# Kernel tuning notes

Measured on AMD Instinct MI355X. Metric: run time of the kernel, lower is better.

The kernel has to match this reference:

```python
import jax, jax.numpy as jnp
import numpy as np

B, L, DIM = 4, 2048, 256
NSETS, PP, POSP, LTMP = 4, 4, 16, 16
PI = float(np.pi)


def setup_inputs() -> dict:
    key = jax.random.key(0)
    ks = jax.random.split(key, 8)
    d = DIM
    return {
        "x": jax.random.normal(ks[0], (B, L, d), jnp.float32),
        "key_proj": jax.random.normal(ks[1], (d, NSETS * PP), jnp.float32) / np.sqrt(d),
        "query_proj": jax.random.normal(ks[2], (d, NSETS * PP), jnp.float32) / np.sqrt(d),
        "ltm_key_proj": jax.random.normal(ks[3], (3 * d, LTMP), jnp.float32) / np.sqrt(3 * d),
        "pos_freqs": jnp.exp(jnp.arange(POSP, dtype=jnp.float32) * (-np.log(10000.0) / POSP)),
        "w_value": jax.random.normal(ks[4], (d, d), jnp.float32) / np.sqrt(d),
        "b_value": jnp.zeros(d, jnp.float32),
        "w_ltm_val": jax.random.normal(ks[5], (d, d), jnp.float32) / np.sqrt(d),
        "b_ltm_val": jnp.zeros(d, jnp.float32),
        "ln_gamma": jnp.ones(d, jnp.float32),
        "ln_beta": jnp.zeros(d, jnp.float32),
        "w_out": jax.random.normal(ks[6], (d, d), jnp.float32) / np.sqrt(d),
        "b_out": jnp.zeros(d, jnp.float32),
        "set_weights": jnp.ones(NSETS, jnp.float32),
        "pos_weight": jnp.ones(1, jnp.float32),
        "surprise_scale": jnp.array(5.0, jnp.float32),
        "surprise_bias": jnp.array(0.0, jnp.float32),
        "resonance_scale": jnp.array(5.0, jnp.float32),
        "resonance_threshold": jnp.array(0.3, jnp.float32),
        "ltm_weight": jnp.array(0.5, jnp.float32),
        "ltm_binding_memory": jnp.zeros((LTMP, d), jnp.complex64),
        "ltm_count": jnp.array(0.0, jnp.float32),
    }


def reference(x, key_proj, query_proj, ltm_key_proj, pos_freqs, w_value, b_value,
              w_ltm_val, b_ltm_val, ln_gamma, ln_beta, w_out, b_out, set_weights,
              pos_weight, surprise_scale, surprise_bias, resonance_scale,
              resonance_threshold, ltm_weight, ltm_binding_memory, ltm_count):
    Bx, Lx, D = x.shape
    # phasor encodings
    key_ph = jnp.exp(1j * (jnp.tanh(x @ key_proj) * PI)).reshape(Bx, Lx, NSETS, PP)
    qry_ph = jnp.exp(1j * (jnp.tanh(x @ query_proj) * PI)).reshape(Bx, Lx, NSETS, PP)
    V_real = x @ w_value + b_value
    weights = jax.nn.softmax(set_weights)
    # joint (cross-bank) phasors
    jk = jnp.prod(key_ph, axis=2)   # [B,L,PP]
    jq = jnp.prod(qry_ph, axis=2)
    # exclusive cumsum of joint keys -> resonance-based surprise write gate
    km = jnp.concatenate([jnp.zeros_like(jk[:, :1]), jnp.cumsum(jk[:, :-1], axis=1)], axis=1)
    rmag = jnp.abs(km * jnp.conj(jq)).mean(-1, keepdims=True)
    posf = jnp.maximum(jnp.arange(Lx, dtype=jnp.float32), 1.0)
    nres = rmag / jnp.sqrt(posf)[None, :, None]
    sc = jnp.clip(resonance_scale, 1.0, 20.0)
    th = jnp.clip(resonance_threshold, 0.1, 0.9)
    surprise = 0.5 * (1.0 - jnp.tanh(sc * (nres - th)))
    gate = jax.nn.sigmoid(surprise_scale * (surprise - 0.5) + surprise_bias)
    Vg = (V_real * gate).astype(jnp.complex64)
    # cross-bank holographic memory (joint key binding)
    cross = jnp.real((jnp.cumsum(jk[..., None] * Vg[:, :, None, :], axis=1)
                      * jnp.conj(jq)[..., None]).sum(2))
    # per-bank holographic memory over all planes
    bound_all = key_ph[..., None] * Vg[:, :, None, None, :]            # [B,L,S,P,D]
    mem_all = jnp.cumsum(bound_all.reshape(Bx, Lx, NSETS * PP, D), axis=1)
    mem_all = mem_all.reshape(Bx, Lx, NSETS, PP, D)
    per_bank = jnp.real((mem_all * jnp.conj(qry_ph)[..., None]).sum(3))  # [B,L,S,D]
    total = (per_bank * weights[None, None, :, None]).sum(2)
    total = (total + cross) / (NSETS + 1.0)
    # positional phasor memory (ungated V)
    pos_ph = jnp.exp(1j * (jnp.arange(Lx, dtype=jnp.float32)[:, None] * pos_freqs * 2.0 * PI))  # [L,P]
    Vc = V_real.astype(jnp.complex64)
    ret_pos = jnp.real((jnp.cumsum(pos_ph[None, :, :, None] * Vc[:, :, None, :], axis=1)
                        * jnp.conj(pos_ph)[None, :, :, None]).sum(2))
    total = 0.5 * total + 0.5 * (jax.nn.sigmoid(pos_weight) * ret_pos)  # fixed_gate = 0.5
    # LTM retrieval from persistent binding memory (detached buffers)
    p1 = jnp.arange(1, Lx + 1, dtype=jnp.float32)[None, :, None]
    rm = jnp.cumsum(x, axis=1) / p1
    rv = jnp.cumsum(x * x, axis=1) / p1 - rm * rm
    rs = jnp.sqrt(jnp.clip(rv, 1e-8, None))
    ltm_ph = jnp.exp(1j * (jnp.tanh(jnp.concatenate([x, rm, rs], -1) @ ltm_key_proj) * PI))  # [B,L,LTMP]
    pers = jnp.real((ltm_binding_memory[None, None] * jnp.conj(ltm_ph)[..., None]).sum(2))
    pnorm = jnp.sqrt(jnp.maximum(ltm_count, 1.0) * LTMP)
    total = total + jax.nn.sigmoid(ltm_weight) * (pers / pnorm)
    # output: LayerNorm + Linear on normalized retrieval, residual
    nrm = jnp.sqrt(jnp.arange(1, Lx + 1, dtype=jnp.float32) * PP)[None, :, None]
    h = total / nrm
    mu = h.mean(-1, keepdims=True)
    var = ((h - mu) ** 2).mean(-1, keepdims=True)
    hn = (h - mu) / jnp.sqrt(var + 1e-5) * ln_gamma + ln_beta
    return x + hn @ w_out + b_out
```

## Files before the change

kernel.cpp:

```cpp
#include <hip/hip_runtime.h>
#include <math.h>

#define B 4
#define L 2048
#define D 256
#define POSP 16
#define LTMP 16
#define T 64
#define C 32
#define F 72
#define PI_F 3.14159274101257324f
#define TWO_PI_D 6.283185307179586476925286766559

__global__ __launch_bounds__(256) void pos_kernel(const float* __restrict__ pos_freqs,
                                                  float* __restrict__ posc,
                                                  float* __restrict__ poss) {
    int idx = blockIdx.x * 256 + threadIdx.x;
    if (idx >= L * POSP) return;
    int t = idx >> 4, p = idx & 15;
    float a = (float)t * pos_freqs[p];
    float th = (a * 2.0f) * PI_F;
    double r = fmod((double)th, TWO_PI_D);
    posc[idx] = (float)cos(r);
    poss[idx] = (float)sin(r);
}

__global__ __launch_bounds__(256) void featurize_kernel(
    const float* __restrict__ x, const float* __restrict__ key_proj,
    const float* __restrict__ query_proj, const float* __restrict__ w_value,
    const float* __restrict__ b_value, const float* __restrict__ set_weights,
    float* __restrict__ V, float* __restrict__ fk, float* __restrict__ fq,
    float* __restrict__ partial) {
    int cg = blockIdx.x;
    int rc = blockIdx.y;
    int b  = blockIdx.z;
    int row0 = rc * 64;
    int tid = threadIdx.x;
    __shared__ float xs[2][32][74];
    __shared__ float ws[2][32][84];
    __shared__ float zbuf[64][20];
    __shared__ float jkv[64][9];
    const bool has_proj = (cg < 2);
    const float* proj = (cg == 0) ? key_proj : query_proj;
    int rg = tid >> 4, cgi = tid & 15;
    int r0 = rg * 4, c0 = cgi * 4;
    int prow = tid >> 2, pc4 = tid & 3;
    float acc[4][4], accp[4];
#pragma unroll
    for (int i = 0; i < 4; i++) {
#pragma unroll
        for (int e = 0; e < 4; e++) acc[i][e] = 0.f;
        accp[i] = 0.f;
    }
    int rrA = tid >> 3, k4A = tid & 7;
    int jA = tid >> 4, c4A = tid & 15;
    float4 xr0, xr1, wr0, wr1, prr;

#define ISSUE_LOADS(kb_)                                                            \
    {                                                                               \
        xr0 = *(const float4*)(x + ((size_t)(b * L + row0 + rrA)) * D + (kb_) + k4A * 4);      \
        xr1 = *(const float4*)(x + ((size_t)(b * L + row0 + 32 + rrA)) * D + (kb_) + k4A * 4); \
        wr0 = *(const float4*)(w_value + (size_t)((kb_) + jA) * D + cg * 64 + c4A * 4);        \
        wr1 = *(const float4*)(w_value + (size_t)((kb_) + 16 + jA) * D + cg * 64 + c4A * 4);   \
        if (has_proj && tid < 128)                                                  \
            prr = *(const float4*)(proj + (size_t)((kb_) + (tid >> 2)) * 16 + (tid & 3) * 4);  \
    }
#define WRITE_LDS(bi)                                                               \
    {                                                                               \
        const float* xp0 = (const float*)&xr0;                                      \
        const float* xp1 = (const float*)&xr1;                                      \
        _Pragma("unroll")                                                           \
        for (int u = 0; u < 4; u++) {                                               \
            xs[bi][k4A * 4 + u][rrA] = xp0[u];                                      \
            xs[bi][k4A * 4 + u][32 + rrA] = xp1[u];                                 \
        }                                                                           \
        *(float4*)&ws[bi][jA][c4A * 4] = wr0;                                       \
        *(float4*)&ws[bi][16 + jA][c4A * 4] = wr1;                                  \
        if (has_proj && tid < 128)                                                  \
            *(float4*)&ws[bi][tid >> 2][64 + (tid & 3) * 4] = prr;                  \
    }

    ISSUE_LOADS(0);
    WRITE_LDS(0);
    __syncthreads();
    for (int kc = 0; kc < 8; kc++) {
        if (kc < 7) ISSUE_LOADS((kc + 1) * 32);
        int bi = kc & 1;
#pragma unroll 8
        for (int j = 0; j < 32; j++) {
            float2 xlo = *(float2*)&xs[bi][j][r0];
            float2 xhi = *(float2*)&xs[bi][j][r0 + 2];
            float4 wv = *(float4*)&ws[bi][j][c0];
            acc[0][0] += xlo.x * wv.x; acc[0][1] += xlo.x * wv.y; acc[0][2] += xlo.x * wv.z; acc[0][3] += xlo.x * wv.w;
            acc[1][0] += xlo.y * wv.x; acc[1][1] += xlo.y * wv.y; acc[1][2] += xlo.y * wv.z; acc[1][3] += xlo.y * wv.w;
            acc[2][0] += xhi.x * wv.x; acc[2][1] += xhi.x * wv.y; acc[2][2] += xhi.x * wv.z; acc[2][3] += xhi.x * wv.w;
            acc[3][0] += xhi.y * wv.x; acc[3][1] += xhi.y * wv.y; acc[3][2] += xhi.y * wv.z; acc[3][3] += xhi.y * wv.w;
            if (has_proj) {
                float xp = xs[bi][j][prow];
                float4 wp = *(float4*)&ws[bi][j][64 + pc4 * 4];
                accp[0] += xp * wp.x; accp[1] += xp * wp.y;
                accp[2] += xp * wp.z; accp[3] += xp * wp.w;
            }
        }
        if (kc < 7) WRITE_LDS((kc + 1) & 1);
        __syncthreads();
    }
#undef ISSUE_LOADS
#undef WRITE_LDS

    {
        int d0 = cg * 64 + c0;
        float4 bv = *(const float4*)(b_value + d0);
#pragma unroll
        for (int i = 0; i < 4; i++) {
            size_t o = ((size_t)(b * L + row0 + r0 + i)) * D + d0;
            *(float4*)(V + o) = make_float4(acc[i][0] + bv.x, acc[i][1] + bv.y,
                                            acc[i][2] + bv.z, acc[i][3] + bv.w);
        }
    }
    if (!has_proj) return;
#pragma unroll
    for (int e = 0; e < 4; e++) zbuf[prow][pc4 * 4 + e] = tanhf(accp[e]) * PI_F;
    __syncthreads();
    {
        int tt = tid >> 2, q = tid & 3;
        size_t bt = (size_t)(b * L + row0 + tt);
        if (cg == 0) {
            float* fp = fk + bt * 40;
#pragma unroll
            for (int e = 0; e < 4; e++) {
                int col = q * 4 + e;
                float si, co; sincosf(zbuf[tt][col], &si, &co);
                fp[2 * col] = co; fp[2 * col + 1] = si;
            }
            float zs = zbuf[tt][q] + zbuf[tt][4 + q] + zbuf[tt][8 + q] + zbuf[tt][12 + q];
            float si, co; sincosf(zs, &si, &co);
            fp[32 + 2 * q] = co; fp[33 + 2 * q] = si;
            jkv[tt][2 * q] = co; jkv[tt][2 * q + 1] = si;
        } else {
            float sw0 = set_weights[0], sw1 = set_weights[1], sw2 = set_weights[2], sw3 = set_weights[3];
            float mx = fmaxf(fmaxf(sw0, sw1), fmaxf(sw2, sw3));
            float e0 = expf(sw0 - mx), e1 = expf(sw1 - mx), e2 = expf(sw2 - mx), e3 = expf(sw3 - mx);
            float esum = e0 + e1 + e2 + e3;
            float wsoft[4] = {e0 / esum, e1 / esum, e2 / esum, e3 / esum};
            float* fp = fq + bt * 40;
#pragma unroll
            for (int e = 0; e < 4; e++) {
                int col = q * 4 + e;
                float si, co; sincosf(zbuf[tt][col], &si, &co);
                float sc = 0.1f * wsoft[col >> 2];
                fp[2 * col] = sc * co; fp[2 * col + 1] = sc * si;
            }
            float zs = zbuf[tt][q] + zbuf[tt][4 + q] + zbuf[tt][8 + q] + zbuf[tt][12 + q];
            float si, co; sincosf(zs, &si, &co);
            fp[32 + 2 * q] = 0.1f * co; fp[33 + 2 * q] = 0.1f * si;
        }
    }
    __syncthreads();
    if (cg == 0) {
        int h = tid >> 7, idxr = tid & 127;
        int rr2 = idxr >> 3, ch = idxr & 7;
#pragma unroll
        for (int s2 = 16; s2 >= 1; s2 >>= 1) {
            if (rr2 < s2) jkv[h * 32 + rr2][ch] += jkv[h * 32 + rr2 + s2][ch];
            __syncthreads();
        }
        if (rr2 == 0) partial[((size_t)(b * 64 + rc * 2 + h)) * 8 + ch] = jkv[h * 32][ch];
    }
}

__global__ __launch_bounds__(512) void gs_scan_kernel(const float* __restrict__ partial,
                                                      float* __restrict__ chunkoff) {
    int b = blockIdx.x;
    int tid = threadIdx.x;
    int c = tid >> 3, ch = tid & 7;
    __shared__ float sc_[64][9];
    float own = partial[((size_t)(b * 64 + c)) * 8 + ch];
    sc_[c][ch] = own;
    __syncthreads();
    for (int off = 1; off < 64; off <<= 1) {
        float v = 0.f;
        if (c >= off) v = sc_[c - off][ch];
        __syncthreads();
        if (c >= off) sc_[c][ch] += v;
        __syncthreads();
    }
    chunkoff[((size_t)(b * 64 + c)) * 8 + ch] = sc_[c][ch] - own;
}

__global__ __launch_bounds__(256) void gs_apply_kernel(
    float* __restrict__ fk, const float* __restrict__ chunkoff,
    const float* __restrict__ surprise_scale, const float* __restrict__ surprise_bias,
    const float* __restrict__ resonance_scale, const float* __restrict__ resonance_threshold) {
    int rc = blockIdx.x, b = blockIdx.y;
    int tid = threadIdx.x;
    int t = tid >> 3, ch = tid & 7;
    __shared__ float sc_[32][9];
    __shared__ float gbuf[32];
    float* fp = fk + ((size_t)(b * L + rc * 32 + t)) * 40;
    float own = fp[32 + ch];
    sc_[t][ch] = own;
    __syncthreads();
    for (int off = 1; off < 32; off <<= 1) {
        float v = 0.f;
        if (t >= off) v = sc_[t - off][ch];
        __syncthreads();
        if (t >= off) sc_[t][ch] += v;
        __syncthreads();
    }
    float run = chunkoff[((size_t)(b * 64 + rc)) * 8 + ch] + sc_[t][ch] - own;
    __syncthreads();
    sc_[t][ch] = run;
    __syncthreads();
    if (tid < 32) {
        int tg = rc * 32 + tid;
        float r0 = sc_[tid][0], r1 = sc_[tid][1], r2 = sc_[tid][2], r3 = sc_[tid][3];
        float r4 = sc_[tid][4], r5 = sc_[tid][5], r6 = sc_[tid][6], r7 = sc_[tid][7];
        float rmag = 0.25f * (sqrtf(r0 * r0 + r1 * r1) + sqrtf(r2 * r2 + r3 * r3) +
                              sqrtf(r4 * r4 + r5 * r5) + sqrtf(r6 * r6 + r7 * r7));
        float scv = fminf(fmaxf(resonance_scale[0], 1.f), 20.f);
        float thv = fminf(fmaxf(resonance_threshold[0], 0.1f), 0.9f);
        float nres = rmag / sqrtf(fmaxf((float)tg, 1.0f));
        float surprise = 0.5f * (1.0f - tanhf(scv * (nres - thv)));
        gbuf[tid] = 1.0f / (1.0f + expf(-(surprise_scale[0] * (surprise - 0.5f) + surprise_bias[0])));
    }
    __syncthreads();
    float gv = gbuf[t];
#pragma unroll
    for (int e = 0; e < 5; e++) fp[ch * 5 + e] *= gv;
}

__global__ __launch_bounds__(256) void stats16_kernel(const float* __restrict__ x,
                                                      float* __restrict__ Sx16,
                                                      float* __restrict__ Sxx16) {
    int s = blockIdx.x, b = blockIdx.y;
    int d = threadIdx.x;
    float sx = 0.f, sxx = 0.f;
#pragma unroll
    for (int k = 0; k < 16; k++) {
        float v = x[((size_t)(b * L + s * 16 + k)) * D + d];
        sx += v; sxx += v * v;
    }
    Sx16[((size_t)(b * 128 + s)) * D + d] = sx;
    Sxx16[((size_t)(b * 128 + s)) * D + d] = sxx;
}

__global__ __launch_bounds__(256) void ltm_z_kernel(
    const float* __restrict__ x, const float* __restrict__ Sx16,
    const float* __restrict__ Sxx16, const float* __restrict__ W,
    float* __restrict__ czsz) {
    int s = blockIdx.x, b = blockIdx.y;
    int tid = threadIdx.x;
    __shared__ float xs[16][257], rms[16][257], rss[16][257];
    float a0 = 0.f, a1 = 0.f, a2 = 0.f, a3 = 0.f;
    float c0 = 0.f, c1 = 0.f, c2 = 0.f, c3 = 0.f;
    int sp = 0;
    for (; sp + 4 <= s; sp += 4) {
        a0 += Sx16[((size_t)(b * 128 + sp)) * D + tid];
        a1 += Sx16[((size_t)(b * 128 + sp + 1)) * D + tid];
        a2 += Sx16[((size_t)(b * 128 + sp + 2)) * D + tid];
        a3 += Sx16[((size_t)(b * 128 + sp + 3)) * D + tid];
        c0 += Sxx16[((size_t)(b * 128 + sp)) * D + tid];
        c1 += Sxx16[((size_t)(b * 128 + sp + 1)) * D + tid];
        c2 += Sxx16[((size_t)(b * 128 + sp + 2)) * D + tid];
        c3 += Sxx16[((size_t)(b * 128 + sp + 3)) * D + tid];
    }
    for (; sp < s; sp++) {
        a0 += Sx16[((size_t)(b * 128 + sp)) * D + tid];
        c0 += Sxx16[((size_t)(b * 128 + sp)) * D + tid];
    }
    float runx = (a0 + a1) + (a2 + a3), runxx = (c0 + c1) + (c2 + c3);
    for (int k = 0; k < 16; k++) {
        int tg = s * 16 + k;
        float xv = x[((size_t)(b * L + tg)) * D + tid];
        runx += xv; runxx += xv * xv;
        float n = (float)(tg + 1);
        float rm = runx / n;
        float rv = runxx / n - rm * rm;
        xs[k][tid] = xv; rms[k][tid] = rm;
        rss[k][tid] = sqrtf(fmaxf(rv, 1e-8f));
    }
    __syncthreads();
    int tl = tid >> 4, p = tid & 15;
    const float* Wp = W + p;
    float u0 = 0.f, u1 = 0.f, u2 = 0.f;
#pragma unroll 4
    for (int j = 0; j < 256; j++) {
        u0 += xs[tl][j] * Wp[j * LTMP];
        u1 += rms[tl][j] * Wp[(256 + j) * LTMP];
        u2 += rss[tl][j] * Wp[(512 + j) * LTMP];
    }
    float z = tanhf(u0 + u1 + u2) * PI_F;
    float si, co; sincosf(z, &si, &co);
    int tg = s * 16 + tl;
    czsz[((size_t)(b * L + tg)) * 32 + p] = co;
    czsz[((size_t)(b * L + tg)) * 32 + 16 + p] = si;
}

__global__ __launch_bounds__(256) void outer_sums_kernel(
    const float* __restrict__ V, const float* __restrict__ fk,
    const float* __restrict__ posc, const float* __restrict__ poss,
    float* __restrict__ S) {
    int g = blockIdx.x;
    int c = blockIdx.y;
    int b = blockIdx.z;
    int tid = threadIdx.x;
    __shared__ float Fk[T][40];
    int F0 = g * 36;
    {
        int t = tid >> 2, q = tid & 3;
        int tg = c * T + t;
        for (int e = 0; e < 9; e++) {
            int fl = q * 9 + e;
            int Fi = F0 + fl;
            float v;
            if (Fi < 40) v = fk[((size_t)(b * L + tg)) * 40 + Fi];
            else {
                int pf = Fi - 40;
                v = (pf & 1) ? poss[tg * POSP + (pf >> 1)] : posc[tg * POSP + (pf >> 1)];
            }
            Fk[t][fl] = v;
        }
    }
    __syncthreads();
    float acc[36];
#pragma unroll
    for (int f = 0; f < 36; f++) acc[f] = 0.f;
    for (int t = 0; t < T; t++) {
        float v = V[((size_t)(b * L + c * T + t)) * D + tid];
#pragma unroll
        for (int f = 0; f < 36; f++) acc[f] += Fk[t][f] * v;
    }
    for (int f = 0; f < 36; f++)
        S[(((size_t)(b * C + c)) * F + F0 + f) * D + tid] = acc[f];
}

__global__ __launch_bounds__(256) void prefix_kernel(float* __restrict__ S) {
    int bf = blockIdx.x;
    int b = bf / F, f = bf % F;
    int d = threadIdx.x;
    size_t base = (((size_t)(b * C)) * F + f) * D + d;
    const size_t stride = (size_t)F * D;
    float v[C];
#pragma unroll
    for (int c = 0; c < C; c++) v[c] = S[base + (size_t)c * stride];
    float run = 0.f;
#pragma unroll
    for (int c = 0; c < C; c++) {
        float t = v[c];
        S[base + (size_t)c * stride] = run;
        run += t;
    }
}

__global__ __launch_bounds__(256) void intra_kernel(
    const float* __restrict__ V, float* __restrict__ ret,
    const float* __restrict__ fk, const float* __restrict__ fq,
    const float* __restrict__ posc, const float* __restrict__ poss,
    const float* __restrict__ Mexc, const float* __restrict__ pos_weight) {
    int tg = blockIdx.x >> 1, dh = blockIdx.x & 1;
    int c = blockIdx.y, b = blockIdx.z;
    int tid = threadIdx.x;
    int t0 = tg * 16;
    __shared__ float Fk[64][76];
    __shared__ float Fq[16][76];
    __shared__ float As[16][68];
    float posq = 0.5f / (1.0f + expf(-pos_weight[0]));
#pragma unroll
    for (int e = 0; e < 18; e++) {
        int idx = e * 256 + tid;
        int r = idx / 72, f = idx - r * 72;
        int tgl = c * T + r;
        float v;
        if (f < 40) v = fk[((size_t)(b * L + tgl)) * 40 + f];
        else { int pf = f - 40; v = (pf & 1) ? poss[tgl * POSP + (pf >> 1)] : posc[tgl * POSP + (pf >> 1)]; }
        Fk[r][f] = v;
    }
#pragma unroll
    for (int e = 0; e < 5; e++) {
        int idx = e * 256 + tid;
        if (idx < 1152) {
            int r = idx / 72, f = idx - r * 72;
            int tgl = c * T + t0 + r;
            float v;
            if (f < 40) v = fq[((size_t)(b * L + tgl)) * 40 + f];
            else { int pf = f - 40; v = posq * ((pf & 1) ? poss[tgl * POSP + (pf >> 1)] : posc[tgl * POSP + (pf >> 1)]); }
            Fq[r][f] = v;
        }
    }
    __syncthreads();
    {
        int r = tid >> 4, k0 = (tid & 15) * 4;
        int tglob = t0 + r;
#pragma unroll
        for (int j = 0; j < 4; j++) {
            int k = k0 + j;
            float a = 0.f;
            if (k <= tglob) {
#pragma unroll
                for (int f = 0; f < F; f++) a += Fq[r][f] * Fk[k][f];
            }
            As[r][k] = a;
        }
    }
    __syncthreads();
    int dl = tid & 127, rowg = tid >> 7;
    int d = dh * 128 + dl;
    int r0 = rowg * 8;
    float acc[8];
#pragma unroll
    for (int i = 0; i < 8; i++) acc[i] = 0.f;
    const float* Mp = Mexc + (((size_t)(b * C + c)) * F) * D + d;
#pragma unroll 8
    for (int f = 0; f < F; f++) {
        float m = Mp[(size_t)f * D];
#pragma unroll
        for (int i = 0; i < 8; i++) acc[i] += Fq[r0 + i][f] * m;
    }
    const float* Vp = V + ((size_t)(b * L + c * T)) * D + d;
    int kmax = t0 + 16;
#pragma unroll 8
    for (int k = 0; k < kmax; k++) {
        float v = Vp[(size_t)k * D];
#pragma unroll
        for (int i = 0; i < 8; i++) acc[i] += As[r0 + i][k] * v;
    }
    float* Rp = ret + ((size_t)(b * L + c * T + t0 + r0)) * D + d;
#pragma unroll
    for (int i = 0; i < 8; i++) Rp[(size_t)i * D] = acc[i];
}

__global__ __launch_bounds__(256) void hprep_kernel(
    const float* __restrict__ retp, const float* __restrict__ czsz,
    const float* __restrict__ ltm_mem, const float* __restrict__ ltm_count,
    const float* __restrict__ ltm_weight, const float* __restrict__ ln_gamma,
    const float* __restrict__ ln_beta, float* __restrict__ hn) {
    int rc = blockIdx.x;
    int b  = blockIdx.y;
    int row0 = rc * 16;
    int tid = threadIdx.x;
    __shared__ float hb[16][260];
    __shared__ float cs[16][33];
    __shared__ float part1[16][17], part2[16][17];
    __shared__ float mu[16], rsig[16];
    float lsig = 1.f / (1.f + expf(-ltm_weight[0]));
    float pnorm = sqrtf(fmaxf(ltm_count[0], 1.f) * (float)LTMP);
    float lcoef = lsig / pnorm;
    float Mre[16], Mim[16];
#pragma unroll
    for (int p = 0; p < 16; p++) {
        Mre[p] = ltm_mem[(p * D + tid) * 2];
        Mim[p] = ltm_mem[(p * D + tid) * 2 + 1];
    }
    float gam = ln_gamma[tid], bet = ln_beta[tid];
#pragma unroll
    for (int e = 0; e < 2; e++) {
        int idx = e * 256 + tid;
        int t = idx >> 5, q = idx & 31;
        cs[t][q] = czsz[((size_t)(b * L + row0 + t)) * 32 + q];
    }
    __syncthreads();
#pragma unroll 4
    for (int t = 0; t < 16; t++) {
        int tg = row0 + t;
        float pers = 0.f;
#pragma unroll
        for (int p = 0; p < 16; p++) pers += Mre[p] * cs[t][p] + Mim[p] * cs[t][16 + p];
        float rv = retp[((size_t)(b * L + tg)) * D + tid];
        hb[t][tid] = (rv + lcoef * pers) / (2.0f * sqrtf((float)(tg + 1)));
    }
    __syncthreads();
    {
        int row = tid & 15, e = tid >> 4;
        float s1 = 0.f, s2 = 0.f;
#pragma unroll
        for (int k = 0; k < 16; k++) {
            float v = hb[row][e + 16 * k];
            s1 += v; s2 += v * v;
        }
        part1[row][e] = s1; part2[row][e] = s2;
    }
    __syncthreads();
    if (tid < 16) {
        float s1 = 0.f, s2 = 0.f;
#pragma unroll
        for (int e = 0; e < 16; e++) { s1 += part1[tid][e]; s2 += part2[tid][e]; }
        float m = s1 / 256.f;
        mu[tid] = m;
        rsig[tid] = rsqrtf(fmaxf(s2 / 256.f - m * m, 0.f) + 1e-5f);
    }
    __syncthreads();
#pragma unroll 4
    for (int t = 0; t < 16; t++)
        hn[((size_t)(b * L + row0 + t)) * D + tid] =
            (hb[t][tid] - mu[t]) * rsig[t] * gam + bet;
}

__global__ __launch_bounds__(256) void gemm_out_kernel(
    const float* __restrict__ hn, const float* __restrict__ w_out,
    const float* __restrict__ b_out, const float* __restrict__ x,
    float* __restrict__ out) {
    int cg = blockIdx.x;
    int rc = blockIdx.y;
    int b  = blockIdx.z;
    int row0 = rc * 64;
    int tid = threadIdx.x;
    __shared__ float hs[2][32][74];
    __shared__ float wo[2][32][68];
    int rg = tid >> 4, cgi = tid & 15;
    int r0 = rg * 4, c0 = cgi * 4;
    float acc[4][4];
#pragma unroll
    for (int i = 0; i < 4; i++)
#pragma unroll
        for (int e = 0; e < 4; e++) acc[i][e] = 0.f;
    int rrA = tid >> 3, k4A = tid & 7;
    int jA = tid >> 4, c4A = tid & 15;
    float4 hr0, hr1, wr0, wr1;

#define ISSUE_LOADS(kb_)                                                            \
    {                                                                               \
        hr0 = *(const float4*)(hn + ((size_t)(b * L + row0 + rrA)) * D + (kb_) + k4A * 4);      \
        hr1 = *(const float4*)(hn + ((size_t)(b * L + row0 + 32 + rrA)) * D + (kb_) + k4A * 4); \
        wr0 = *(const float4*)(w_out + (size_t)((kb_) + jA) * D + cg * 64 + c4A * 4);           \
        wr1 = *(const float4*)(w_out + (size_t)((kb_) + 16 + jA) * D + cg * 64 + c4A * 4);      \
    }
#define WRITE_LDS(bi)                                                               \
    {                                                                               \
        const float* hp0 = (const float*)&hr0;                                      \
        const float* hp1 = (const float*)&hr1;                                      \
        _Pragma("unroll")                                                           \
        for (int u = 0; u < 4; u++) {                                               \
            hs[bi][k4A * 4 + u][rrA] = hp0[u];                                      \
            hs[bi][k4A * 4 + u][32 + rrA] = hp1[u];                                 \
        }                                                                           \
        *(float4*)&wo[bi][jA][c4A * 4] = wr0;                                       \
        *(float4*)&wo[bi][16 + jA][c4A * 4] = wr1;                                  \
    }

    ISSUE_LOADS(0);
    WRITE_LDS(0);
    __syncthreads();
    for (int kc = 0; kc < 8; kc++) {
        if (kc < 7) ISSUE_LOADS((kc + 1) * 32);
        int bi = kc & 1;
#pragma unroll 8
        for (int j = 0; j < 32; j++) {
            float2 xlo = *(float2*)&hs[bi][j][r0];
            float2 xhi = *(float2*)&hs[bi][j][r0 + 2];
            float4 wv = *(float4*)&wo[bi][j][c0];
            acc[0][0] += xlo.x * wv.x; acc[0][1] += xlo.x * wv.y; acc[0][2] += xlo.x * wv.z; acc[0][3] += xlo.x * wv.w;
            acc[1][0] += xlo.y * wv.x; acc[1][1] += xlo.y * wv.y; acc[1][2] += xlo.y * wv.z; acc[1][3] += xlo.y * wv.w;
            acc[2][0] += xhi.x * wv.x; acc[2][1] += xhi.x * wv.y; acc[2][2] += xhi.x * wv.z; acc[2][3] += xhi.x * wv.w;
            acc[3][0] += xhi.y * wv.x; acc[3][1] += xhi.y * wv.y; acc[3][2] += xhi.y * wv.z; acc[3][3] += xhi.y * wv.w;
        }
        if (kc < 7) WRITE_LDS((kc + 1) & 1);
        __syncthreads();
    }
#undef ISSUE_LOADS
#undef WRITE_LDS
    {
        int d0 = cg * 64 + c0;
        float4 bo = *(const float4*)(b_out + d0);
#pragma unroll
        for (int i = 0; i < 4; i++) {
            size_t o = ((size_t)(b * L + row0 + r0 + i)) * D + d0;
            float4 xa = *(const float4*)(x + o);
            *(float4*)(out + o) = make_float4(xa.x + acc[i][0] + bo.x, xa.y + acc[i][1] + bo.y,
                                              xa.z + acc[i][2] + bo.z, xa.w + acc[i][3] + bo.w);
        }
    }
}

extern "C" void kernel_launch(void* const* d_in, const int* in_sizes, int n_in,
                              void* d_out, int out_size, void* d_ws, size_t ws_size,
                              hipStream_t stream) {
    (void)in_sizes; (void)n_in; (void)out_size; (void)ws_size;
    const float* x            = (const float*)d_in[0];
    const float* key_proj     = (const float*)d_in[1];
    const float* query_proj   = (const float*)d_in[2];
    const float* ltm_key_proj = (const float*)d_in[3];
    const float* pos_freqs    = (const float*)d_in[4];
    const float* w_value      = (const float*)d_in[5];
    const float* b_value      = (const float*)d_in[6];
    const float* ln_gamma     = (const float*)d_in[9];
    const float* ln_beta      = (const float*)d_in[10];
    const float* w_out        = (const float*)d_in[11];
    const float* b_out        = (const float*)d_in[12];
    const float* set_weights  = (const float*)d_in[13];
    const float* pos_weight   = (const float*)d_in[14];
    const float* surprise_scale      = (const float*)d_in[15];
    const float* surprise_bias       = (const float*)d_in[16];
    const float* resonance_scale     = (const float*)d_in[17];
    const float* resonance_threshold = (const float*)d_in[18];
    const float* ltm_weight   = (const float*)d_in[19];
    const float* ltm_mem      = (const float*)d_in[20];
    const float* ltm_count    = (const float*)d_in[21];
    float* out = (float*)d_out;

    float* ws = (float*)d_ws;
    size_t off = 0;
    float* V     = ws + off; off += (size_t)B * L * D;
    float* ret   = ws + off; off += (size_t)B * L * D;
    float* fk    = ws + off; off += (size_t)B * L * 40;
    float* fq    = ws + off; off += (size_t)B * L * 40;
    float* posc  = ws + off; off += (size_t)L * POSP;
    float* poss  = ws + off; off += (size_t)L * POSP;
    float* Sx16  = ws + off; off += (size_t)B * 128 * D;
    float* Sxx16 = ws + off; off += (size_t)B * 128 * D;
    float* czsz  = ws + off; off += (size_t)B * L * 32;
    float* S     = ws + off; off += (size_t)B * C * F * D;
    float* partial  = ws + off; off += (size_t)B * 64 * 8;
    float* chunkoff = ws + off; off += (size_t)B * 64 * 8;
    float* hn = V;

    pos_kernel<<<dim3(128), 256, 0, stream>>>(pos_freqs, posc, poss);
    featurize_kernel<<<dim3(4, 32, B), 256, 0, stream>>>(x, key_proj, query_proj, w_value,
                                                         b_value, set_weights, V, fk, fq, partial);
    gs_scan_kernel<<<dim3(B), 512, 0, stream>>>(partial, chunkoff);
    gs_apply_kernel<<<dim3(64, B), 256, 0, stream>>>(fk, chunkoff, surprise_scale, surprise_bias,
                                                     resonance_scale, resonance_threshold);
    stats16_kernel<<<dim3(128, B), 256, 0, stream>>>(x, Sx16, Sxx16);
    ltm_z_kernel<<<dim3(128, B), 256, 0, stream>>>(x, Sx16, Sxx16, ltm_key_proj, czsz);
    outer_sums_kernel<<<dim3(2, C, B), 256, 0, stream>>>(V, fk, posc, poss, S);
    prefix_kernel<<<dim3(B * F), 256, 0, stream>>>(S);
    intra_kernel<<<dim3(8, C, B), 256, 0, stream>>>(V, ret, fk, fq, posc, poss, S, pos_weight);
    hprep_kernel<<<dim3(128, B), 256, 0, stream>>>(ret, czsz, ltm_mem, ltm_count, ltm_weight,
                                                   ln_gamma, ln_beta, hn);
    gemm_out_kernel<<<dim3(4, 32, B), 256, 0, stream>>>(hn, w_out, b_out, x, out);
}
```

Measured before the change: 253.9 us.

## Split outer-sum chunks in halves, transpose LTM weights, vectorize shared-memory dot products

The LTM key projection is transposed into a workspace buffer inside pos_kernel, so ltm_z_kernel can read weights and padded shared rows with float4 loads. outer_sums_kernel now splits each 64-step chunk into two 32-step halves, doubling its grid for more parallelism, and prefix_kernel adds the two halves while scanning. The intra_kernel score dot product and the outer-sum inner loop also use float4 shared loads. This adds an extra workspace buffer and doubles the outer-sum write traffic.

```diff
diff --git a/kernel.cpp b/kernel.cpp
--- a/kernel.cpp
+++ b/kernel.cpp
@@ -13,16 +13,25 @@
 #define TWO_PI_D 6.283185307179586476925286766559
 
 __global__ __launch_bounds__(256) void pos_kernel(const float* __restrict__ pos_freqs,
+                                                  const float* __restrict__ lkp,
                                                   float* __restrict__ posc,
-                                                  float* __restrict__ poss) {
+                                                  float* __restrict__ poss,
+                                                  float* __restrict__ Wt) {
     int idx = blockIdx.x * 256 + threadIdx.x;
-    if (idx >= L * POSP) return;
-    int t = idx >> 4, p = idx & 15;
-    float a = (float)t * pos_freqs[p];
-    float th = (a * 2.0f) * PI_F;
-    double r = fmod((double)th, TWO_PI_D);
-    posc[idx] = (float)cos(r);
-    poss[idx] = (float)sin(r);
+    if (idx < L * POSP) {
+        int t = idx >> 4, p = idx & 15;
+        float a = (float)t * pos_freqs[p];
+        float th = (a * 2.0f) * PI_F;
+        double r = fmod((double)th, TWO_PI_D);
+        posc[idx] = (float)cos(r);
+        poss[idx] = (float)sin(r);
+    } else {
+        int i2 = idx - L * POSP;
+        if (i2 < 16 * 768) {
+            int p = i2 / 768, j = i2 - p * 768;
+            Wt[i2] = lkp[j * 16 + p];
+        }
+    }
 }
 
 __global__ __launch_bounds__(256) void featurize_kernel(
@@ -247,11 +256,11 @@
 
 __global__ __launch_bounds__(256) void ltm_z_kernel(
     const float* __restrict__ x, const float* __restrict__ Sx16,
-    const float* __restrict__ Sxx16, const float* __restrict__ W,
+    const float* __restrict__ Sxx16, const float* __restrict__ Wt,
     float* __restrict__ czsz) {
     int s = blockIdx.x, b = blockIdx.y;
     int tid = threadIdx.x;
-    __shared__ float xs[16][257], rms[16][257], rss[16][257];
+    __shared__ float xs[16][260], rms[16][260], rss[16][260];
     float a0 = 0.f, a1 = 0.f, a2 = 0.f, a3 = 0.f;
     float c0 = 0.f, c1 = 0.f, c2 = 0.f, c3 = 0.f;
     int sp = 0;
@@ -282,13 +291,19 @@
     }
     __syncthreads();
     int tl = tid >> 4, p = tid & 15;
-    const float* Wp = W + p;
+    const float* W0 = Wt + p * 768;
     float u0 = 0.f, u1 = 0.f, u2 = 0.f;
 #pragma unroll 4
-    for (int j = 0; j < 256; j++) {
-        u0 += xs[tl][j] * Wp[j * LTMP];
-        u1 += rms[tl][j] * Wp[(256 + j) * LTMP];
-        u2 += rss[tl][j] * Wp[(512 + j) * LTMP];
+    for (int j4 = 0; j4 < 64; j4++) {
+        float4 xv = *(float4*)&xs[tl][j4 * 4];
+        float4 wx = *(const float4*)(W0 + j4 * 4);
+        float4 rv = *(float4*)&rms[tl][j4 * 4];
+        float4 wr = *(const float4*)(W0 + 256 + j4 * 4);
+        float4 sv = *(float4*)&rss[tl][j4 * 4];
+        float4 wz = *(const float4*)(W0 + 512 + j4 * 4);
+        u0 += xv.x * wx.x + xv.y * wx.y + xv.z * wx.z + xv.w * wx.w;
+        u1 += rv.x * wr.x + rv.y * wr.y + rv.z * wr.z + rv.w * wr.w;
+        u2 += sv.x * wz.x + sv.y * wz.y + sv.z * wz.z + sv.w * wz.w;
     }
     float z = tanhf(u0 + u1 + u2) * PI_F;
     float si, co; sincosf(z, &si, &co);
@@ -300,24 +315,27 @@
 __global__ __launch_bounds__(256) void outer_sums_kernel(
     const float* __restrict__ V, const float* __restrict__ fk,
     const float* __restrict__ posc, const float* __restrict__ poss,
-    float* __restrict__ S) {
-    int g = blockIdx.x;
+    float* __restrict__ Sh) {
+    int g = blockIdx.x >> 1, h = blockIdx.x & 1;
     int c = blockIdx.y;
     int b = blockIdx.z;
     int tid = threadIdx.x;
-    __shared__ float Fk[T][40];
+    __shared__ float Fk[32][40];
     int F0 = g * 36;
     {
-        int t = tid >> 2, q = tid & 3;
-        int tg = c * T + t;
-        for (int e = 0; e < 9; e++) {
-            int fl = q * 9 + e;
-            int Fi = F0 + fl;
-            float v;
-            if (Fi < 40) v = fk[((size_t)(b * L + tg)) * 40 + Fi];
-            else {
-                int pf = Fi - 40;
-                v = (pf & 1) ? poss[tg * POSP + (pf >> 1)] : posc[tg * POSP + (pf >> 1)];
+        int t = tid >> 3, q = tid & 7;
+        int tg = c * T + h * 32 + t;
+#pragma unroll
+        for (int e = 0; e < 5; e++) {
+            int fl = q * 5 + e;
+            float v = 0.f;
+            if (fl < 36) {
+                int Fi = F0 + fl;
+                if (Fi < 40) v = fk[((size_t)(b * L + tg)) * 40 + Fi];
+                else {
+                    int pf = Fi - 40;
+                    v = (pf & 1) ? poss[tg * POSP + (pf >> 1)] : posc[tg * POSP + (pf >> 1)];
+                }
             }
             Fk[t][fl] = v;
         }
@@ -326,30 +344,37 @@
     float acc[36];
 #pragma unroll
     for (int f = 0; f < 36; f++) acc[f] = 0.f;
-    for (int t = 0; t < T; t++) {
-        float v = V[((size_t)(b * L + c * T + t)) * D + tid];
-#pragma unroll
-        for (int f = 0; f < 36; f++) acc[f] += Fk[t][f] * v;
+    for (int t = 0; t < 32; t++) {
+        float v = V[((size_t)(b * L + c * T + h * 32 + t)) * D + tid];
+#pragma unroll
+        for (int f4 = 0; f4 < 9; f4++) {
+            float4 fkv = *(float4*)&Fk[t][f4 * 4];
+            acc[f4 * 4 + 0] += fkv.x * v;
+            acc[f4 * 4 + 1] += fkv.y * v;
+            acc[f4 * 4 + 2] += fkv.z * v;
+            acc[f4 * 4 + 3] += fkv.w * v;
+        }
     }
     for (int f = 0; f < 36; f++)
-        S[(((size_t)(b * C + c)) * F + F0 + f) * D + tid] = acc[f];
-}
-
-__global__ __launch_bounds__(256) void prefix_kernel(float* __restrict__ S) {
+        Sh[((((size_t)(b * C + c)) * 2 + h) * F + F0 + f) * D + tid] = acc[f];
+}
+
+__global__ __launch_bounds__(256) void prefix_kernel(const float* __restrict__ Sh,
+                                                     float* __restrict__ S) {
     int bf = blockIdx.x;
     int b = bf / F, f = bf % F;
     int d = threadIdx.x;
-    size_t base = (((size_t)(b * C)) * F + f) * D + d;
-    const size_t stride = (size_t)F * D;
-    float v[C];
-#pragma unroll
-    for (int c = 0; c < C; c++) v[c] = S[base + (size_t)c * stride];
+    float v0[C], v1[C];
+#pragma unroll
+    for (int c = 0; c < C; c++) {
+        v0[c] = Sh[((((size_t)(b * C + c)) * 2 + 0) * F + f) * D + d];
+        v1[c] = Sh[((((size_t)(b * C + c)) * 2 + 1) * F + f) * D + d];
+    }
     float run = 0.f;
 #pragma unroll
     for (int c = 0; c < C; c++) {
-        float t = v[c];
-        S[base + (size_t)c * stride] = run;
-        run += t;
+        S[(((size_t)(b * C + c)) * F + f) * D + d] = run;
+        run += v0[c] + v1[c];
     }
 }
 
@@ -398,7 +423,11 @@
             float a = 0.f;
             if (k <= tglob) {
 #pragma unroll
-                for (int f = 0; f < F; f++) a += Fq[r][f] * Fk[k][f];
+                for (int f4 = 0; f4 < 18; f4++) {
+                    float4 q = *(float4*)&Fq[r][f4 * 4];
+                    float4 kk = *(float4*)&Fk[k][f4 * 4];
+                    a += q.x * kk.x + q.y * kk.y + q.z * kk.z + q.w * kk.w;
+                }
             }
             As[r][k] = a;
         }
@@ -609,21 +638,23 @@
     float* Sx16  = ws + off; off += (size_t)B * 128 * D;
     float* Sxx16 = ws + off; off += (size_t)B * 128 * D;
     float* czsz  = ws + off; off += (size_t)B * L * 32;
+    float* Sh    = ws + off; off += (size_t)B * C * 2 * F * D;
     float* S     = ws + off; off += (size_t)B * C * F * D;
     float* partial  = ws + off; off += (size_t)B * 64 * 8;
     float* chunkoff = ws + off; off += (size_t)B * 64 * 8;
+    float* Wt    = ws + off; off += (size_t)16 * 768;
     float* hn = V;
 
-    pos_kernel<<<dim3(128), 256, 0, stream>>>(pos_freqs, posc, poss);
+    pos_kernel<<<dim3(176), 256, 0, stream>>>(pos_freqs, ltm_key_proj, posc, poss, Wt);
     featurize_kernel<<<dim3(4, 32, B), 256, 0, stream>>>(x, key_proj, query_proj, w_value,
                                                          b_value, set_weights, V, fk, fq, partial);
     gs_scan_kernel<<<dim3(B), 512, 0, stream>>>(partial, chunkoff);
     gs_apply_kernel<<<dim3(64, B), 256, 0, stream>>>(fk, chunkoff, surprise_scale, surprise_bias,
                                                      resonance_scale, resonance_threshold);
     stats16_kernel<<<dim3(128, B), 256, 0, stream>>>(x, Sx16, Sxx16);
-    ltm_z_kernel<<<dim3(128, B), 256, 0, stream>>>(x, Sx16, Sxx16, ltm_key_proj, czsz);
-    outer_sums_kernel<<<dim3(2, C, B), 256, 0, stream>>>(V, fk, posc, poss, S);
-    prefix_kernel<<<dim3(B * F), 256, 0, stream>>>(S);
+    ltm_z_kernel<<<dim3(128, B), 256, 0, stream>>>(x, Sx16, Sxx16, Wt, czsz);
+    outer_sums_kernel<<<dim3(4, C, B), 256, 0, stream>>>(V, fk, posc, poss, Sh);
+    prefix_kernel<<<dim3(B * F), 256, 0, stream>>>(Sh, S);
     intra_kernel<<<dim3(8, C, B), 256, 0, stream>>>(V, ret, fk, fq, posc, poss, S, pos_weight);
     hprep_kernel<<<dim3(128, B), 256, 0, stream>>>(ret, czsz, ltm_mem, ltm_count, ltm_weight,
                                                    ln_gamma, ln_beta, hn);
```

Result: slower. 281.9 us (+11.0%).
